# Kernel optimization log

Hardware: AMD Instinct MI355X
Metric: run time of the kernel (lower is better)

The kernel has to match this reference:

```python
import jax, jax.numpy as jnp
import numpy as np

N_NODES = 50000
N_EDGES = 800000
NODE_DIM = 128
EDGE_DIM = 16
HIDDEN = 64


def _gcn_conv(x, W, b, src, dst, n_nodes):
    """PyG-style GCNConv: add self-loops, symmetric deg^-1/2 normalization,
    aggregate messages from src into dst, then add bias. x: [N, Fin]."""
    h = x @ W  # [N, Fout]
    loops = jnp.arange(n_nodes)
    s = jnp.concatenate([src, loops])  # sources incl. self-loops
    d = jnp.concatenate([dst, loops])  # targets incl. self-loops
    deg = jax.ops.segment_sum(jnp.ones_like(d, dtype=h.dtype), d, num_segments=n_nodes)
    dinv = jax.lax.rsqrt(jnp.maximum(deg, 1.0))  # deg >= 1 thanks to self-loops
    norm = dinv[s] * dinv[d]  # [E+N]
    msg = h[s] * norm[:, None]  # gather + scale
    out = jax.ops.segment_sum(msg, d, num_segments=n_nodes)  # scatter-add
    return out + b


def setup_inputs() -> dict:
    key = jax.random.key(0)
    ks = jax.random.split(key, 12)
    x = jax.random.normal(ks[0], (N_NODES, NODE_DIM), dtype=jnp.float32)
    edge_index = jax.random.randint(ks[1], (2, N_EDGES), 0, N_NODES, dtype=jnp.int64)
    edge_attr = jax.random.normal(ks[2], (N_EDGES, EDGE_DIM), dtype=jnp.float32)
    def glorot(k, fan_in, fan_out):
        s = float(np.sqrt(2.0 / (fan_in + fan_out)))
        return jax.random.normal(k, (fan_in, fan_out), dtype=jnp.float32) * s
    W1 = glorot(ks[3], NODE_DIM, HIDDEN)
    b1 = jnp.zeros((HIDDEN,), jnp.float32)
    W2 = glorot(ks[4], HIDDEN, HIDDEN)
    b2 = jnp.zeros((HIDDEN,), jnp.float32)
    Wm1 = glorot(ks[5], 2 * HIDDEN + EDGE_DIM, HIDDEN)
    bm1 = jnp.zeros((HIDDEN,), jnp.float32)
    Wm2 = glorot(ks[6], HIDDEN, 2)
    bm2 = jnp.zeros((2,), jnp.float32)
    return {"x": x, "edge_index": edge_index, "edge_attr": edge_attr,
            "W1": W1, "b1": b1, "W2": W2, "b2": b2,
            "Wm1": Wm1, "bm1": bm1, "Wm2": Wm2, "bm2": bm2}


def reference(x, edge_index, edge_attr, W1, b1, W2, b2, Wm1, bm1, Wm2, bm2):
    n = x.shape[0]
    src, dst = edge_index[0], edge_index[1]
    h = jax.nn.relu(_gcn_conv(x, W1, b1, src, dst, n))
    h = jax.nn.relu(_gcn_conv(h, W2, b2, src, dst, n))
    # gather endpoint embeddings + concat edge features -> edge MLP
    edge_embed = jnp.concatenate([h[src], h[dst], edge_attr], axis=1)  # [E, 2H+Fe]
    out = jax.nn.relu(edge_embed @ Wm1 + bm1) @ Wm2 + bm2  # [E, 2]
    return out
```

## Files before the change

kernel.cpp:

```cpp
#include <hip/hip_runtime.h>
#include <hip/hip_fp16.h>


typedef float v4f __attribute__((ext_vector_type(4)));
typedef _Float16 v4h __attribute__((ext_vector_type(4)));

__device__ __forceinline__ void fma4(float4& a, float s, const float4& b) {
    a.x = fmaf(s, b.x, a.x);
    a.y = fmaf(s, b.y, a.y);
    a.z = fmaf(s, b.z, a.z);
    a.w = fmaf(s, b.w, a.w);
}

__device__ __forceinline__ float4 relu4(float4 v) {
    v.x = fmaxf(v.x, 0.f); v.y = fmaxf(v.y, 0.f);
    v.z = fmaxf(v.z, 0.f); v.w = fmaxf(v.w, 0.f);
    return v;
}

__device__ __forceinline__ void store4(float* C, size_t idx, float4 v) {
    *reinterpret_cast<float4*>(C + idx) = v;
}
__device__ __forceinline__ void store4(__half* C, size_t idx, float4 v) {
    __half2 lo = __floats2half2_rn(v.x, v.y);
    __half2 hi = __floats2half2_rn(v.z, v.w);
    uint2 raw;
    raw.x = *reinterpret_cast<unsigned*>(&lo);
    raw.y = *reinterpret_cast<unsigned*>(&hi);
    *reinterpret_cast<uint2*>(C + idx) = raw;
}

__device__ __forceinline__ void load_lds16(const void* g, void* l) {
    __builtin_amdgcn_global_load_lds(
        (const __attribute__((address_space(1))) void*)g,
        (__attribute__((address_space(3))) void*)l, 16, 0, 0);
}

__global__ void k_count(const int* __restrict__ dst, int* __restrict__ cnt,
                        int* __restrict__ rank, int E) {
    int e = blockIdx.x * 256 + threadIdx.x;
    if (e < E) rank[e] = atomicAdd(&cnt[dst[e]], 1);
}

__global__ void k_bsum(const int* __restrict__ cnt, int* __restrict__ bsum,
                       float* __restrict__ dinv, int N) {
    int i = blockIdx.x * 256 + threadIdx.x;
    int v = (i < N) ? cnt[i] : 0;
    if (i < N) dinv[i] = rsqrtf((float)v + 1.0f);
    int r = v;
#pragma unroll
    for (int d = 1; d < 64; d <<= 1) r += __shfl_xor(r, d);
    __shared__ int ws[4];
    if ((threadIdx.x & 63) == 0) ws[threadIdx.x >> 6] = r;
    __syncthreads();
    if (threadIdx.x == 0) bsum[blockIdx.x] = ws[0] + ws[1] + ws[2] + ws[3];
}

__global__ void k_scanb(int* __restrict__ bsum, int nb) {
    int t = threadIdx.x;
    int lane = t & 63, w = t >> 6;
    int v = (t < nb) ? bsum[t] : 0;
    int x = v;
#pragma unroll
    for (int d = 1; d < 64; d <<= 1) {
        int y = __shfl_up(x, d);
        if (lane >= d) x += y;
    }
    __shared__ int ws[4];
    if (lane == 63) ws[w] = x;
    __syncthreads();
    int woff = 0;
    for (int j = 0; j < w; j++) woff += ws[j];
    if (t < nb) bsum[t] = woff + x - v;
}

__global__ void k_scan3(const int* __restrict__ cnt, const int* __restrict__ bsum,
                        int* __restrict__ row_ptr, int N, int E) {
    int t = threadIdx.x, b = blockIdx.x;
    int i = b * 256 + t;
    int lane = t & 63, w = t >> 6;
    int v = (i < N) ? cnt[i] : 0;
    int x = v;
#pragma unroll
    for (int d = 1; d < 64; d <<= 1) {
        int y = __shfl_up(x, d);
        if (lane >= d) x += y;
    }
    __shared__ int ws[4];
    if (lane == 63) ws[w] = x;
    __syncthreads();
    int woff = 0;
    for (int j = 0; j < w; j++) woff += ws[j];
    if (i < N) row_ptr[i] = bsum[b] + woff + x - v;
    if (i == 0) row_ptr[N] = E;
}

__global__ void k_fill(const int* __restrict__ src, const int* __restrict__ dst,
                       const int* __restrict__ row_ptr, const int* __restrict__ rank,
                       int* __restrict__ csr_src, int E) {
    int e = blockIdx.x * 256 + threadIdx.x;
    if (e >= E) return;
    csr_src[row_ptr[dst[e]] + rank[e]] = src[e];
}

template<int K, bool RELU_A, bool SCALE, typename OutT>
__global__ __launch_bounds__(256) void k_gemm(const float* __restrict__ A,
                                              const float* __restrict__ B,
                                              const float* __restrict__ dinv,
                                              OutT* __restrict__ C, int M) {
    constexpr int AS = K + 4;
    __shared__ float As[32 * AS];
    __shared__ float Bs[64 * 64];
    const int t = threadIdx.x;
    const int r0 = blockIdx.x * 32;

    constexpr int C4 = K / 4;
    for (int idx = t; idx < 32 * C4; idx += 256) {
        int row = idx / C4, c4 = idx % C4;
        float4 v = make_float4(0.f, 0.f, 0.f, 0.f);
        if (r0 + row < M)
            v = reinterpret_cast<const float4*>(A + (size_t)(r0 + row) * K)[c4];
        if (RELU_A) v = relu4(v);
        *reinterpret_cast<float4*>(&As[row * AS + 4 * c4]) = v;
    }

    const int tx = t & 15, ty = t >> 4;
    float4 acc[2];
    acc[0] = acc[1] = make_float4(0.f, 0.f, 0.f, 0.f);

    for (int c = 0; c < K / 64; c++) {
        __syncthreads();
        for (int idx = t; idx < 64 * 16; idx += 256)
            reinterpret_cast<float4*>(Bs)[idx] =
                reinterpret_cast<const float4*>(B + (size_t)c * 64 * 64)[idx];
        __syncthreads();
#pragma unroll 4
        for (int k0 = 0; k0 < 64; k0 += 4) {
            float4 b0 = *reinterpret_cast<const float4*>(&Bs[(k0 + 0) * 64 + 4 * tx]);
            float4 b1 = *reinterpret_cast<const float4*>(&Bs[(k0 + 1) * 64 + 4 * tx]);
            float4 b2 = *reinterpret_cast<const float4*>(&Bs[(k0 + 2) * 64 + 4 * tx]);
            float4 b3 = *reinterpret_cast<const float4*>(&Bs[(k0 + 3) * 64 + 4 * tx]);
#pragma unroll
            for (int i = 0; i < 2; i++) {
                float4 a = *reinterpret_cast<const float4*>(
                    &As[(2 * ty + i) * AS + c * 64 + k0]);
                fma4(acc[i], a.x, b0);
                fma4(acc[i], a.y, b1);
                fma4(acc[i], a.z, b2);
                fma4(acc[i], a.w, b3);
            }
        }
    }

#pragma unroll
    for (int i = 0; i < 2; i++) {
        int row = r0 + 2 * ty + i;
        if (row < M) {
            float4 o = acc[i];
            if (SCALE) {
                float di = dinv[row];
                o = make_float4(di * o.x, di * o.y, di * o.z, di * o.w);
            }
            store4(C, (size_t)row * 64 + 4 * tx, o);
        }
    }
}

__global__ __launch_bounds__(256) void k_proj(const float* __restrict__ A,
                                              const float* __restrict__ B0,
                                              const float* __restrict__ B1,
                                              const float* __restrict__ bias,
                                              __half* __restrict__ C0,
                                              __half* __restrict__ C1, int M) {
    constexpr int AS = 68;
    __shared__ float As[32 * AS];
    __shared__ float Bs[64 * 64];
    const int t = threadIdx.x;
    const int r0 = blockIdx.x * 32;

    for (int idx = t; idx < 32 * 16; idx += 256) {
        int row = idx / 16, c4 = idx % 16;
        float4 v = make_float4(0.f, 0.f, 0.f, 0.f);
        if (r0 + row < M)
            v = relu4(reinterpret_cast<const float4*>(A + (size_t)(r0 + row) * 64)[c4]);
        *reinterpret_cast<float4*>(&As[row * AS + 4 * c4]) = v;
    }

    const int tx = t & 15, ty = t >> 4;
    const float4 bb = *reinterpret_cast<const float4*>(&bias[4 * tx]);
    for (int m = 0; m < 2; m++) {
        const float* B = m ? B1 : B0;
        __half* C = m ? C1 : C0;
        __syncthreads();
        for (int idx = t; idx < 64 * 16; idx += 256)
            reinterpret_cast<float4*>(Bs)[idx] =
                reinterpret_cast<const float4*>(B)[idx];
        __syncthreads();
        float4 acc[2];
        acc[0] = acc[1] = make_float4(0.f, 0.f, 0.f, 0.f);
#pragma unroll 4
        for (int k0 = 0; k0 < 64; k0 += 4) {
            float4 b0 = *reinterpret_cast<const float4*>(&Bs[(k0 + 0) * 64 + 4 * tx]);
            float4 b1 = *reinterpret_cast<const float4*>(&Bs[(k0 + 1) * 64 + 4 * tx]);
            float4 b2 = *reinterpret_cast<const float4*>(&Bs[(k0 + 2) * 64 + 4 * tx]);
            float4 b3 = *reinterpret_cast<const float4*>(&Bs[(k0 + 3) * 64 + 4 * tx]);
#pragma unroll
            for (int i = 0; i < 2; i++) {
                float4 a = *reinterpret_cast<const float4*>(&As[(2 * ty + i) * AS + k0]);
                fma4(acc[i], a.x, b0);
                fma4(acc[i], a.y, b1);
                fma4(acc[i], a.z, b2);
                fma4(acc[i], a.w, b3);
            }
        }
#pragma unroll
        for (int i = 0; i < 2; i++) {
            int row = r0 + 2 * ty + i;
            if (row < M) {
                float4 o = acc[i];
                if (m == 0) {
                    o.x += bb.x; o.y += bb.y; o.z += bb.z; o.w += bb.w;
                }
                store4(C, (size_t)row * 64 + 4 * tx, o);
            }
        }
    }
}

__global__ __launch_bounds__(256, 4) void k_agg(const __half* __restrict__ A16,
                                                const int* __restrict__ row_ptr,
                                                const int* __restrict__ csr_src,
                                                const float* __restrict__ dinv,
                                                const float* __restrict__ bias,
                                                float* __restrict__ out, int N) {
    int gw = (blockIdx.x * 256 + threadIdx.x) >> 6;
    int sub = (threadIdx.x >> 4) & 3;
    int l = threadIdx.x & 15;
    int node = gw * 4 + sub;
    if (node >= N) return;
    const uint2* A4 = reinterpret_cast<const uint2*>(A16);

    int beg = row_ptr[node], end = row_ptr[node + 1];
    uint2 selfv = A4[(size_t)node * 16 + l];
    float2 a0 = __half22float2(*reinterpret_cast<__half2*>(&selfv.x));
    float2 a1 = __half22float2(*reinterpret_cast<__half2*>(&selfv.y));
    float4 acc = make_float4(a0.x, a0.y, a1.x, a1.y);

#define ACC(u)                                                          \
    {                                                                   \
        float2 f0 = __half22float2(*reinterpret_cast<__half2*>(&u.x));  \
        float2 f1 = __half22float2(*reinterpret_cast<__half2*>(&u.y));  \
        acc.x += f0.x; acc.y += f0.y; acc.z += f1.x; acc.w += f1.y;     \
    }
    for (int p = beg; p < end; p += 16) {
        int m = min(16, end - p);
        int sl = (p + l < end) ? csr_src[p + l] : 0;
        int j = 0;
        for (; j + 7 < m; j += 8) {
            uint2 u0 = A4[(size_t)__shfl(sl, j + 0, 16) * 16 + l];
            uint2 u1 = A4[(size_t)__shfl(sl, j + 1, 16) * 16 + l];
            uint2 u2 = A4[(size_t)__shfl(sl, j + 2, 16) * 16 + l];
            uint2 u3 = A4[(size_t)__shfl(sl, j + 3, 16) * 16 + l];
            uint2 u4 = A4[(size_t)__shfl(sl, j + 4, 16) * 16 + l];
            uint2 u5 = A4[(size_t)__shfl(sl, j + 5, 16) * 16 + l];
            uint2 u6 = A4[(size_t)__shfl(sl, j + 6, 16) * 16 + l];
            uint2 u7 = A4[(size_t)__shfl(sl, j + 7, 16) * 16 + l];
            ACC(u0) ACC(u1) ACC(u2) ACC(u3) ACC(u4) ACC(u5) ACC(u6) ACC(u7)
        }
        for (; j + 3 < m; j += 4) {
            uint2 u0 = A4[(size_t)__shfl(sl, j + 0, 16) * 16 + l];
            uint2 u1 = A4[(size_t)__shfl(sl, j + 1, 16) * 16 + l];
            uint2 u2 = A4[(size_t)__shfl(sl, j + 2, 16) * 16 + l];
            uint2 u3 = A4[(size_t)__shfl(sl, j + 3, 16) * 16 + l];
            ACC(u0) ACC(u1) ACC(u2) ACC(u3)
        }
        for (; j < m; j++) {
            uint2 u0 = A4[(size_t)__shfl(sl, j, 16) * 16 + l];
            ACC(u0)
        }
    }
#undef ACC
    float di = dinv[node];
    float4 bb = *reinterpret_cast<const float4*>(&bias[4 * l]);
    float4 o = make_float4(fmaf(di, acc.x, bb.x), fmaf(di, acc.y, bb.y),
                           fmaf(di, acc.z, bb.z), fmaf(di, acc.w, bb.w));
    *reinterpret_cast<float4*>(&out[(size_t)node * 64 + 4 * l]) = o;
}

__global__ __launch_bounds__(256, 4) void k_edge(
    const __half* __restrict__ Ps, const __half* __restrict__ Pd,
    const int* __restrict__ src, const int* __restrict__ dst,
    const float* __restrict__ ea, const float* __restrict__ We,
    const float* __restrict__ Wm2, const float* __restrict__ bm2,
    float* __restrict__ out, int E) {
    __shared__ __align__(16) char smem[4 * 8192];
    const int lane = threadIdx.x & 63;
    const int wid = (blockIdx.x * 256 + threadIdx.x) >> 6;
    const int li = lane & 15, g = lane >> 4;
    const int e0 = wid * 64;
    if (e0 >= E) return;

    char* wbase = smem + (threadIdx.x >> 6) * 8192;
    const float4* ea4 = reinterpret_cast<const float4*>(ea);

    v4h af[4];
#pragma unroll
    for (int m = 0; m < 4; m++) {
        v4h a;
#pragma unroll
        for (int i = 0; i < 4; i++)
            a[i] = (_Float16)We[(4 * g + i) * 64 + 16 * m + li];
        af[m] = a;
    }

    float4 w2lo[4], w2hi[4];
#pragma unroll
    for (int m = 0; m < 4; m++) {
        int dim0 = 16 * m + 4 * g;
        w2lo[m] = *reinterpret_cast<const float4*>(&Wm2[2 * dim0]);
        w2hi[m] = *reinterpret_cast<const float4*>(&Wm2[2 * dim0 + 4]);
    }
    const float c0 = bm2[0], c1 = bm2[1];

    const int ecl = min(e0 + lane, E - 1);
    const int sv = src[ecl], dv = dst[ecl];

    const int jrow = lane >> 3;
    const int csw = (lane & 7) ^ jrow;

#define STAGE(n, b)                                                              \
    {                                                                            \
        char* lb = wbase + (b) * 4096 + lane * 16;                               \
        int n0 = __shfl(sv, 16 * (n) + jrow);                                    \
        int n1 = __shfl(sv, 16 * (n) + 8 + jrow);                                \
        int n2 = __shfl(dv, 16 * (n) + jrow);                                    \
        int n3 = __shfl(dv, 16 * (n) + 8 + jrow);                                \
        load_lds16((const char*)Ps + (size_t)n0 * 128 + (csw << 4), lb);         \
        load_lds16((const char*)Ps + (size_t)n1 * 128 + (csw << 4), lb + 1024);  \
        load_lds16((const char*)Pd + (size_t)n2 * 128 + (csw << 4), lb + 2048);  \
        load_lds16((const char*)Pd + (size_t)n3 * 128 + (csw << 4), lb + 3072);  \
    }

    STAGE(0, 0)

    v4h bh[4];
#pragma unroll
    for (int n = 0; n < 4; n++) {
        int ee = min(e0 + 16 * n + li, E - 1);
        float4 bf = ea4[(size_t)ee * 4 + g];
        v4h t;
        t[0] = (_Float16)bf.x; t[1] = (_Float16)bf.y;
        t[2] = (_Float16)bf.z; t[3] = (_Float16)bf.w;
        bh[n] = t;
    }

#pragma unroll
    for (int n = 0; n < 4; n++) {
        if (n < 3) STAGE(n + 1, (n + 1) & 1)
        if (n < 3) asm volatile("s_waitcnt vmcnt(4)" ::: "memory");
        else       asm volatile("s_waitcnt vmcnt(0)" ::: "memory");

        const char* rb = wbase + (n & 1) * 4096;
        uint2 us[4], ud[4];
#pragma unroll
        for (int m = 0; m < 4; m++) {
            int q = 4 * m + g;
            int off = li * 128 + ((((q >> 1) ^ (li & 7)) << 4) | ((q & 1) << 3));
            us[m] = *reinterpret_cast<const uint2*>(rb + off);
            ud[m] = *reinterpret_cast<const uint2*>(rb + 2048 + off);
        }

        float p0 = 0.f, p1 = 0.f;
#pragma unroll
        for (int m = 0; m < 4; m++) {
            float2 s0 = __half22float2(*reinterpret_cast<__half2*>(&us[m].x));
            float2 s1 = __half22float2(*reinterpret_cast<__half2*>(&us[m].y));
            float2 d0 = __half22float2(*reinterpret_cast<__half2*>(&ud[m].x));
            float2 d1 = __half22float2(*reinterpret_cast<__half2*>(&ud[m].y));
            v4f c;
            c[0] = s0.x + d0.x;
            c[1] = s0.y + d0.y;
            c[2] = s1.x + d1.x;
            c[3] = s1.y + d1.y;
            v4f q = __builtin_amdgcn_mfma_f32_16x16x16f16(af[m], bh[n], c, 0, 0, 0);
            float u0 = fmaxf(q[0], 0.f), u1 = fmaxf(q[1], 0.f);
            float u2 = fmaxf(q[2], 0.f), u3 = fmaxf(q[3], 0.f);
            p0 += u0 * w2lo[m].x + u1 * w2lo[m].z + u2 * w2hi[m].x + u3 * w2hi[m].z;
            p1 += u0 * w2lo[m].y + u1 * w2lo[m].w + u2 * w2hi[m].y + u3 * w2hi[m].w;
        }
        p0 += __shfl_xor(p0, 16); p0 += __shfl_xor(p0, 32);
        p1 += __shfl_xor(p1, 16); p1 += __shfl_xor(p1, 32);
        const int e = e0 + 16 * n + li;
        if (g == 0 && e < E) {
            *reinterpret_cast<float2*>(&out[(size_t)e * 2]) =
                make_float2(p0 + c0, p1 + c1);
        }
    }
#undef STAGE
}

static inline size_t align256(size_t x) { return (x + 255) & ~(size_t)255; }

extern "C" void kernel_launch(void* const* d_in, const int* in_sizes, int n_in,
                              void* d_out, int out_size, void* d_ws, size_t ws_size,
                              hipStream_t stream) {
    const float* x = (const float*)d_in[0];
    const int* ei = (const int*)d_in[1];
    const float* ea = (const float*)d_in[2];
    const float* W1 = (const float*)d_in[3];
    const float* b1 = (const float*)d_in[4];
    const float* W2 = (const float*)d_in[5];
    const float* b2 = (const float*)d_in[6];
    const float* Wm1 = (const float*)d_in[7];
    const float* bm1 = (const float*)d_in[8];
    const float* Wm2 = (const float*)d_in[9];
    const float* bm2 = (const float*)d_in[10];

    const int N = in_sizes[0] / 128;
    const int E = in_sizes[1] / 2;
    const int* src = ei;
    const int* dst = ei + E;
    float* out = (float*)d_out;

    const int NB = (N + 255) / 256;

    char* p = (char*)d_ws;
    int* cnt = (int*)p;        p += align256((size_t)N * 4);
    int* rank = (int*)p;       p += align256((size_t)E * 4);
    int* row_ptr = (int*)p;    p += align256((size_t)(N + 1) * 4);
    int* bsum = (int*)p;       p += align256((size_t)NB * 4);
    int* csr_src = (int*)p;    p += align256((size_t)E * 4);
    float* dinv = (float*)p;   p += align256((size_t)N * 4);
    __half* A16 = (__half*)p;  p += align256((size_t)N * 64 * 2);
    float* B = (float*)p;      p += align256((size_t)N * 64 * 4);
    __half* Ps16 = (__half*)p; p += align256((size_t)N * 64 * 2);
    __half* Pd16 = (__half*)p;

    hipMemsetAsync(cnt, 0, (size_t)N * sizeof(int), stream);
    k_count<<<(E + 255) / 256, 256, 0, stream>>>(dst, cnt, rank, E);
    k_bsum<<<NB, 256, 0, stream>>>(cnt, bsum, dinv, N);
    k_scanb<<<1, 256, 0, stream>>>(bsum, NB);
    k_scan3<<<NB, 256, 0, stream>>>(cnt, bsum, row_ptr, N, E);
    k_fill<<<(E + 255) / 256, 256, 0, stream>>>(src, dst, row_ptr, rank, csr_src, E);

    k_gemm<128, false, true, __half><<<(N + 31) / 32, 256, 0, stream>>>(
        x, W1, dinv, A16, N);
    k_agg<<<(N + 15) / 16, 256, 0, stream>>>(A16, row_ptr, csr_src, dinv, b1, B, N);

    k_gemm<64, true, true, __half><<<(N + 31) / 32, 256, 0, stream>>>(
        B, W2, dinv, A16, N);
    k_agg<<<(N + 15) / 16, 256, 0, stream>>>(A16, row_ptr, csr_src, dinv, b2, B, N);

    k_proj<<<(N + 31) / 32, 256, 0, stream>>>(B, Wm1, Wm1 + 64 * 64, bm1,
                                              Ps16, Pd16, N);
    int waves = (E + 63) / 64;
    k_edge<<<(waves + 3) / 4, 256, 0, stream>>>(Ps16, Pd16, src, dst, ea,
                                                Wm1 + 128 * 64, Wm2, bm2,
                                                out, E);
}
```

Baseline: 289.1 us.

## Triple-buffer the edge kernel's LDS gather to prefetch two stages ahead

The edge MLP kernel now gives each wave three 4 KB LDS buffers instead of two, and issues the gathers for stages 0–2 before the first compute, so two stages of node-embedding rows are in flight. The vmcnt waits change to match. The edge_attr loads move ahead of the first gather, and output stores are deferred to the end so they no longer sit in the vmcnt queue between stages. The aim is to hide more gather latency. In exchange, shared memory per block grows to 48 KB, which may cut resident blocks per CU below the launch-bounds target.

```diff
diff --git a/kernel.cpp b/kernel.cpp
--- a/kernel.cpp
+++ b/kernel.cpp
@@ -293,14 +293,14 @@
     const float* __restrict__ ea, const float* __restrict__ We,
     const float* __restrict__ Wm2, const float* __restrict__ bm2,
     float* __restrict__ out, int E) {
-    __shared__ __align__(16) char smem[4 * 8192];
+    __shared__ __align__(16) char smem[4 * 12288];
     const int lane = threadIdx.x & 63;
     const int wid = (blockIdx.x * 256 + threadIdx.x) >> 6;
     const int li = lane & 15, g = lane >> 4;
     const int e0 = wid * 64;
     if (e0 >= E) return;
 
-    char* wbase = smem + (threadIdx.x >> 6) * 8192;
+    char* wbase = smem + (threadIdx.x >> 6) * 12288;
     const float4* ea4 = reinterpret_cast<const float4*>(ea);
 
     v4h af[4];
@@ -324,6 +324,17 @@
 
     const int ecl = min(e0 + lane, E - 1);
     const int sv = src[ecl], dv = dst[ecl];
+
+    v4h bh[4];
+#pragma unroll
+    for (int n = 0; n < 4; n++) {
+        int ee = min(e0 + 16 * n + li, E - 1);
+        float4 bf = ea4[(size_t)ee * 4 + g];
+        v4h t;
+        t[0] = (_Float16)bf.x; t[1] = (_Float16)bf.y;
+        t[2] = (_Float16)bf.z; t[3] = (_Float16)bf.w;
+        bh[n] = t;
+    }
 
     const int jrow = lane >> 3;
     const int csw = (lane & 7) ^ jrow;
@@ -341,62 +352,66 @@
         load_lds16((const char*)Pd + (size_t)n3 * 128 + (csw << 4), lb + 3072);  \
     }
 
+    float p0s[4], p1s[4];
+
+#define COMPUTE(n, b)                                                             \
+    {                                                                             \
+        const char* rb = wbase + (b) * 4096;                                      \
+        uint2 us[4], ud[4];                                                       \
+        _Pragma("unroll")                                                         \
+        for (int m = 0; m < 4; m++) {                                             \
+            int q = 4 * m + g;                                                    \
+            int off = li * 128 + ((((q >> 1) ^ (li & 7)) << 4) | ((q & 1) << 3)); \
+            us[m] = *reinterpret_cast<const uint2*>(rb + off);                    \
+            ud[m] = *reinterpret_cast<const uint2*>(rb + 2048 + off);             \
+        }                                                                         \
+        float p0 = 0.f, p1 = 0.f;                                                 \
+        _Pragma("unroll")                                                         \
+        for (int m = 0; m < 4; m++) {                                             \
+            float2 s0 = __half22float2(*reinterpret_cast<__half2*>(&us[m].x));    \
+            float2 s1 = __half22float2(*reinterpret_cast<__half2*>(&us[m].y));    \
+            float2 d0 = __half22float2(*reinterpret_cast<__half2*>(&ud[m].x));    \
+            float2 d1 = __half22float2(*reinterpret_cast<__half2*>(&ud[m].y));    \
+            v4f c;                                                                \
+            c[0] = s0.x + d0.x;                                                   \
+            c[1] = s0.y + d0.y;                                                   \
+            c[2] = s1.x + d1.x;                                                   \
+            c[3] = s1.y + d1.y;                                                   \
+            v4f q = __builtin_amdgcn_mfma_f32_16x16x16f16(af[m], bh[n], c, 0, 0, 0); \
+            float u0 = fmaxf(q[0], 0.f), u1 = fmaxf(q[1], 0.f);                   \
+            float u2 = fmaxf(q[2], 0.f), u3 = fmaxf(q[3], 0.f);                   \
+            p0 += u0 * w2lo[m].x + u1 * w2lo[m].z + u2 * w2hi[m].x + u3 * w2hi[m].z; \
+            p1 += u0 * w2lo[m].y + u1 * w2lo[m].w + u2 * w2hi[m].y + u3 * w2hi[m].w; \
+        }                                                                         \
+        p0 += __shfl_xor(p0, 16); p0 += __shfl_xor(p0, 32);                       \
+        p1 += __shfl_xor(p1, 16); p1 += __shfl_xor(p1, 32);                       \
+        p0s[n] = p0; p1s[n] = p1;                                                 \
+    }
+
     STAGE(0, 0)
-
-    v4h bh[4];
-#pragma unroll
-    for (int n = 0; n < 4; n++) {
-        int ee = min(e0 + 16 * n + li, E - 1);
-        float4 bf = ea4[(size_t)ee * 4 + g];
-        v4h t;
-        t[0] = (_Float16)bf.x; t[1] = (_Float16)bf.y;
-        t[2] = (_Float16)bf.z; t[3] = (_Float16)bf.w;
-        bh[n] = t;
-    }
-
-#pragma unroll
-    for (int n = 0; n < 4; n++) {
-        if (n < 3) STAGE(n + 1, (n + 1) & 1)
-        if (n < 3) asm volatile("s_waitcnt vmcnt(4)" ::: "memory");
-        else       asm volatile("s_waitcnt vmcnt(0)" ::: "memory");
-
-        const char* rb = wbase + (n & 1) * 4096;
-        uint2 us[4], ud[4];
-#pragma unroll
-        for (int m = 0; m < 4; m++) {
-            int q = 4 * m + g;
-            int off = li * 128 + ((((q >> 1) ^ (li & 7)) << 4) | ((q & 1) << 3));
-            us[m] = *reinterpret_cast<const uint2*>(rb + off);
-            ud[m] = *reinterpret_cast<const uint2*>(rb + 2048 + off);
-        }
-
-        float p0 = 0.f, p1 = 0.f;
-#pragma unroll
-        for (int m = 0; m < 4; m++) {
-            float2 s0 = __half22float2(*reinterpret_cast<__half2*>(&us[m].x));
-            float2 s1 = __half22float2(*reinterpret_cast<__half2*>(&us[m].y));
-            float2 d0 = __half22float2(*reinterpret_cast<__half2*>(&ud[m].x));
-            float2 d1 = __half22float2(*reinterpret_cast<__half2*>(&ud[m].y));
-            v4f c;
-            c[0] = s0.x + d0.x;
-            c[1] = s0.y + d0.y;
-            c[2] = s1.x + d1.x;
-            c[3] = s1.y + d1.y;
-            v4f q = __builtin_amdgcn_mfma_f32_16x16x16f16(af[m], bh[n], c, 0, 0, 0);
-            float u0 = fmaxf(q[0], 0.f), u1 = fmaxf(q[1], 0.f);
-            float u2 = fmaxf(q[2], 0.f), u3 = fmaxf(q[3], 0.f);
-            p0 += u0 * w2lo[m].x + u1 * w2lo[m].z + u2 * w2hi[m].x + u3 * w2hi[m].z;
-            p1 += u0 * w2lo[m].y + u1 * w2lo[m].w + u2 * w2hi[m].y + u3 * w2hi[m].w;
-        }
-        p0 += __shfl_xor(p0, 16); p0 += __shfl_xor(p0, 32);
-        p1 += __shfl_xor(p1, 16); p1 += __shfl_xor(p1, 32);
-        const int e = e0 + 16 * n + li;
-        if (g == 0 && e < E) {
-            *reinterpret_cast<float2*>(&out[(size_t)e * 2]) =
-                make_float2(p0 + c0, p1 + c1);
-        }
-    }
+    STAGE(1, 1)
+    STAGE(2, 2)
+    asm volatile("s_waitcnt vmcnt(8)" ::: "memory");
+    COMPUTE(0, 0)
+    STAGE(3, 0)
+    asm volatile("s_waitcnt vmcnt(8)" ::: "memory");
+    COMPUTE(1, 1)
+    asm volatile("s_waitcnt vmcnt(4)" ::: "memory");
+    COMPUTE(2, 2)
+    asm volatile("s_waitcnt vmcnt(0)" ::: "memory");
+    COMPUTE(3, 0)
 #undef STAGE
+#undef COMPUTE
+
+    if (g == 0) {
+#pragma unroll
+        for (int n = 0; n < 4; n++) {
+            int e = e0 + 16 * n + li;
+            if (e < E)
+                *reinterpret_cast<float2*>(&out[(size_t)e * 2]) =
+                    make_float2(p0s[n] + c0, p1s[n] + c1);
+        }
+    }
 }
 
 static inline size_t align256(size_t x) { return (x + 255) & ~(size_t)255; }
```

New measurement: 289.7 us. No clear change (+0.2%).
